# Kernel tuning notes

Hardware: AMD Instinct MI355X
Metric: run time of the kernel (lower is better)

The kernel has to match this reference:

```python
import jax, jax.numpy as jnp
import numpy as np

NUM_EMBEDDINGS = 8192
EMBEDDING_DIM = 256


def setup_inputs() -> dict:
    key = jax.random.key(0)
    k1, k2 = jax.random.split(key)
    z = jax.random.normal(k1, (8, 4096, EMBEDDING_DIM), dtype=jnp.float32)
    # stand-in for orthogonally-initialized nn.Embedding weight
    codebook = jax.random.normal(k2, (NUM_EMBEDDINGS, EMBEDDING_DIM), dtype=jnp.float32)
    return {"z": z, "codebook": codebook}


def reference(z, codebook):
    # z: [..., D], codebook: [K, D]
    zf = z.reshape(-1, EMBEDDING_DIM)                      # [N, D]
    # squared-euclidean distances via ||z||^2 + ||e||^2 - 2 z.e^T
    distances = (
        jnp.sum(zf * zf, axis=1, keepdims=True)            # [N, 1]
        + jnp.sum(codebook * codebook, axis=1)             # [K]
        - 2.0 * jnp.matmul(zf, codebook.T)                 # [N, K]
    )
    encoding_indices = jnp.argmin(distances, axis=1)[:, None]  # [N, 1]
    quantized = codebook[encoding_indices[:, 0]]           # [N, D] gather
    quantized = quantized.reshape(z.shape)
    return quantized, encoding_indices
```

## Files before the change

### kernel.cpp

```cpp
#include <hip/hip_runtime.h>
#include <cfloat>
#include <stdint.h>

#define NROWS   32768
#define NCODES  8192
#define KDIM    256
#define QOUT_OFFSET (NROWS * KDIM)

#define BM      64
#define BN      256
#define NQ      4
#define CODES_Q (NCODES / NQ)
#define NKC     (KDIM / 32)
#define NIT     (CODES_Q / BN * NKC)
#define THREADS 256

#define BPAN 8192
#define BBUF (2 * BPAN)
#define ALDS_SPLIT 32768

typedef __bf16 bf16x4 __attribute__((ext_vector_type(4)));
typedef __bf16 bf16x8 __attribute__((ext_vector_type(8)));
typedef float  f32x4  __attribute__((ext_vector_type(4)));

__global__ void vq_panel_kernel(const float* __restrict__ cb,
                                char* __restrict__ cbP,
                                float* __restrict__ cnorm) {
    const int t    = threadIdx.x;
    const int row  = t >> 2;
    const int seg  = t & 3;
    const int code = blockIdx.x * 64 + row;
    const int cl   = code & 127;
    const int pt   = code >> 7;
    const float4* cb4 = (const float4*)cb;

    float ssq = 0.f;
    #pragma unroll
    for (int i = 0; i < 16; ++i) {
        int f = seg * 16 + i;
        float4 v = cb4[(size_t)code * 64 + f];
        int k   = f * 4;
        int kc  = k >> 5;
        int kl  = k & 31;
        int oct = kl >> 3;
        int rem = kl & 7;
        bf16x4 h, l;
        float xs[4] = {v.x, v.y, v.z, v.w};
        #pragma unroll
        for (int e = 0; e < 4; ++e) {
            __bf16 hh = (__bf16)xs[e];
            h[e] = hh;
            l[e] = (__bf16)(xs[e] - (float)hh);
            ssq  = fmaf(xs[e], xs[e], ssq);
        }
        int lanefrag = (oct << 4) | (cl & 15);
        char* base = cbP + ((size_t)(pt * NKC + kc)) * BBUF
                         + ((cl >> 4) * 64 + lanefrag) * 16 + rem * 2;
        *(bf16x4*)base          = h;
        *(bf16x4*)(base + BPAN) = l;
    }
    ssq += __shfl_xor(ssq, 1, 64);
    ssq += __shfl_xor(ssq, 2, 64);
    if (seg == 0) cnorm[code] = ssq;
}

__global__ __launch_bounds__(THREADS, 2) void vq_main_kernel(
        const float* __restrict__ z, const char* __restrict__ cbP,
        const float* __restrict__ cnorm,
        float* __restrict__ partD, int* __restrict__ partI) {

    __shared__ __align__(16) char Alds[2 * ALDS_SPLIT];

    const int t     = threadIdx.x;
    const int wave  = t >> 6;
    const int lane  = t & 63;
    const int l15   = lane & 15;
    const int q     = blockIdx.x >> 9;
    const int row0  = (blockIdx.x & 511) * BM;
    const int qcode = q * CODES_Q;
    const int qp16  = q * 16;

    const float4* z4 = (const float4*)z;

    f32x4 acc[4][4];
    float mv[16];
    int   mi[16];
    #pragma unroll
    for (int i = 0; i < 4; ++i)
        #pragma unroll
        for (int j = 0; j < 4; ++j)
            acc[i][j] = (f32x4){0.f, 0.f, 0.f, 0.f};
    #pragma unroll
    for (int s = 0; s < 16; ++s) { mv[s] = FLT_MAX; mi[s] = 0; }

    {
        const int arow = t >> 2;
        const int aseg = t & 3;
        #pragma unroll
        for (int p = 0; p < 8; ++p) {
            float4 f0 = z4[(size_t)(row0 + arow) * 64 + aseg * 16 + 2 * p];
            float4 f1 = z4[(size_t)(row0 + arow) * 64 + aseg * 16 + 2 * p + 1];
            float xs[8] = {f0.x, f0.y, f0.z, f0.w, f1.x, f1.y, f1.z, f1.w};
            bf16x8 hv, lv;
            #pragma unroll
            for (int e = 0; e < 8; ++e) {
                __bf16 hh = (__bf16)xs[e];
                hv[e] = hh;
                lv[e] = (__bf16)(xs[e] - (float)hh);
            }
            int kc  = aseg * 2 + (p >> 2);
            int oct = p & 3;
            int slot = ((kc * 4 + (arow >> 4)) * 64 + (oct << 4) + (arow & 15)) * 16;
            *(bf16x8*)(Alds + slot)              = hv;
            *(bf16x8*)(Alds + ALDS_SPLIT + slot) = lv;
        }
    }

    bf16x8 B0h[4], B0l[4], B1h[4], B1l[4];
    #pragma unroll
    for (int j = 0; j < 4; ++j) {
        int g16 = wave * 4 + j;
        const char* pb = cbP + ((size_t)(qp16 + (g16 >> 3)) * 8 + 0) * BBUF
                             + ((g16 & 7) * 64 + lane) * 16;
        B0h[j] = *(const bf16x8*)pb;
        B0l[j] = *(const bf16x8*)(pb + BPAN);
    }

    __syncthreads();

#define VQ_BODY(N, CURH, CURL, NXTH, NXTL)                                    \
    {                                                                         \
        const int ct = (N) >> 3, kc = (N) & 7;                                \
        const int np = (N) + 1;                                               \
        if (np < NIT) {                                                       \
            const int ct1 = np >> 3, kc1 = np & 7;                            \
            _Pragma("unroll")                                                 \
            for (int j = 0; j < 4; ++j) {                                     \
                int g16 = ct1 * 16 + wave * 4 + j;                            \
                const char* pb = cbP                                          \
                    + ((size_t)(qp16 + (g16 >> 3)) * 8 + kc1) * BBUF          \
                    + ((g16 & 7) * 64 + lane) * 16;                           \
                NXTH[j] = *(const bf16x8*)pb;                                 \
                NXTL[j] = *(const bf16x8*)(pb + BPAN);                        \
            }                                                                 \
        }                                                                     \
        bf16x8 ah[4], al[4];                                                  \
        _Pragma("unroll")                                                     \
        for (int i = 0; i < 4; ++i) {                                         \
            int sl = ((kc * 4 + i) * 64 + lane) * 16;                         \
            ah[i] = *(const bf16x8*)(Alds + sl);                              \
            al[i] = *(const bf16x8*)(Alds + ALDS_SPLIT + sl);                 \
        }                                                                     \
        _Pragma("unroll")                                                     \
        for (int i = 0; i < 4; ++i)                                           \
            _Pragma("unroll")                                                 \
            for (int j = 0; j < 4; ++j)                                       \
                acc[i][j] = __builtin_amdgcn_mfma_f32_16x16x32_bf16(          \
                                ah[i], CURH[j], acc[i][j], 0, 0, 0);          \
        _Pragma("unroll")                                                     \
        for (int i = 0; i < 4; ++i)                                           \
            _Pragma("unroll")                                                 \
            for (int j = 0; j < 4; ++j)                                       \
                acc[i][j] = __builtin_amdgcn_mfma_f32_16x16x32_bf16(          \
                                ah[i], CURL[j], acc[i][j], 0, 0, 0);          \
        _Pragma("unroll")                                                     \
        for (int i = 0; i < 4; ++i)                                           \
            _Pragma("unroll")                                                 \
            for (int j = 0; j < 4; ++j)                                       \
                acc[i][j] = __builtin_amdgcn_mfma_f32_16x16x32_bf16(          \
                                al[i], CURH[j], acc[i][j], 0, 0, 0);          \
        if (kc == 7) {                                                        \
            _Pragma("unroll")                                                 \
            for (int j = 0; j < 4; ++j) {                                     \
                int code = qcode + (ct * 16 + wave * 4 + j) * 16 + l15;       \
                float cn = cnorm[code];                                       \
                _Pragma("unroll")                                             \
                for (int i = 0; i < 4; ++i) {                                 \
                    _Pragma("unroll")                                         \
                    for (int r = 0; r < 4; ++r) {                             \
                        float d = fmaf(-2.f, acc[i][j][r], cn);               \
                        int s = i * 4 + r;                                    \
                        if (d < mv[s]) { mv[s] = d; mi[s] = code; }           \
                    }                                                         \
                    acc[i][j] = (f32x4){0.f, 0.f, 0.f, 0.f};                  \
                }                                                             \
            }                                                                 \
        }                                                                     \
    }

    for (int n = 0; n < NIT; n += 2) {
        VQ_BODY(n,     B0h, B0l, B1h, B1l)
        VQ_BODY(n + 1, B1h, B1l, B0h, B0l)
    }
#undef VQ_BODY

    #pragma unroll
    for (int s = 0; s < 16; ++s) {
        #pragma unroll
        for (int m = 1; m <= 8; m <<= 1) {
            float ov = __shfl_xor(mv[s], m, 64);
            int   oi = __shfl_xor(mi[s], m, 64);
            if (ov < mv[s] || (ov == mv[s] && oi < mi[s])) { mv[s] = ov; mi[s] = oi; }
        }
    }
    __syncthreads();
    float* redV = (float*)Alds;
    int*   redI = (int*)(Alds + 4 * BM * 4);
    if (l15 == 0) {
        int qq = lane >> 4;
        #pragma unroll
        for (int i = 0; i < 4; ++i)
            #pragma unroll
            for (int r = 0; r < 4; ++r) {
                int ml = i * 16 + qq * 4 + r;
                redV[wave * BM + ml] = mv[i * 4 + r];
                redI[wave * BM + ml] = mi[i * 4 + r];
            }
    }
    __syncthreads();
    if (t < BM) {
        float bv = redV[t];
        int   bi = redI[t];
        #pragma unroll
        for (int w = 1; w < 4; ++w) {
            float v  = redV[w * BM + t];
            int   id = redI[w * BM + t];
            if (v < bv || (v == bv && id < bi)) { bv = v; bi = id; }
        }
        partD[(size_t)q * NROWS + row0 + t] = bv;
        partI[(size_t)q * NROWS + row0 + t] = bi;
    }
}

__global__ void vq_merge_kernel(const float* __restrict__ partD,
                                const int* __restrict__ partI,
                                float* __restrict__ idx_out) {
    const int row = blockIdx.x * 256 + threadIdx.x;
    float bv = partD[row];
    int   bi = partI[row];
    #pragma unroll
    for (int q = 1; q < NQ; ++q) {
        float v  = partD[(size_t)q * NROWS + row];
        int   id = partI[(size_t)q * NROWS + row];
        if (v < bv || (v == bv && id < bi)) { bv = v; bi = id; }
    }
    idx_out[row] = (float)bi;
}

__global__ void vq_gather_kernel(const float* __restrict__ cb,
                                 const float* __restrict__ idx_f,
                                 float* __restrict__ quant) {
    const int t   = threadIdx.x;
    const int row = blockIdx.x * 64 + (t >> 2);
    const int seg = t & 3;
    const int best = (int)idx_f[row];
    const float4* src = (const float4*)cb + (size_t)best * (KDIM / 4);
    float4* dst = (float4*)quant + (size_t)row * (KDIM / 4);
    #pragma unroll
    for (int i = 0; i < 16; ++i)
        dst[seg * 16 + i] = src[seg * 16 + i];
}

extern "C" void kernel_launch(void* const* d_in, const int* in_sizes, int n_in,
                              void* d_out, int out_size, void* d_ws, size_t ws_size,
                              hipStream_t stream) {
    const float* z  = (const float*)d_in[0];
    const float* cb = (const float*)d_in[1];
    float* quant   = (float*)d_out;
    float* idx_out = (float*)d_out + QOUT_OFFSET;
    float* cnorm   = (float*)d_ws;
    char*  cbP     = (char*)d_out;
    float* partD   = (float*)((char*)d_out + 8 * 1024 * 1024);
    int*   partI   = (int*)((char*)d_out + 8 * 1024 * 1024 + NQ * NROWS * 4);

    vq_panel_kernel<<<NCODES / 64, 256, 0, stream>>>(cb, cbP, cnorm);
    vq_main_kernel<<<NQ * (NROWS / BM), THREADS, 0, stream>>>(z, cbP, cnorm, partD, partI);
    vq_merge_kernel<<<NROWS / 256, 256, 0, stream>>>(partD, partI, idx_out);
    vq_gather_kernel<<<NROWS / 64, 256, 0, stream>>>(cb, idx_out, quant);
}
```

Measured before the change: 423.7 us.

## Double-buffer A fragments from LDS and prefetch codebook norms early

```diff
diff --git a/kernel.cpp b/kernel.cpp
--- a/kernel.cpp
+++ b/kernel.cpp
@@ -79,6 +79,8 @@
     const int row0  = (blockIdx.x & 511) * BM;
     const int qcode = q * CODES_Q;
     const int qp16  = q * 16;
+    const int wp    = wave >> 1;
+    const int bvoff = ((wave & 1) * 256 + lane) * 16;
 
     const float4* z4 = (const float4*)z;
 
@@ -117,63 +119,84 @@
     }
 
     bf16x8 B0h[4], B0l[4], B1h[4], B1l[4];
-    #pragma unroll
-    for (int j = 0; j < 4; ++j) {
-        int g16 = wave * 4 + j;
-        const char* pb = cbP + ((size_t)(qp16 + (g16 >> 3)) * 8 + 0) * BBUF
-                             + ((g16 & 7) * 64 + lane) * 16;
-        B0h[j] = *(const bf16x8*)pb;
-        B0l[j] = *(const bf16x8*)(pb + BPAN);
+    {
+        const char* pb  = cbP + ((size_t)(qp16 + wp) * 8) * BBUF + bvoff;
+        const char* pbl = pb + BPAN;
+        #pragma unroll
+        for (int j = 0; j < 4; ++j) {
+            B0h[j] = *(const bf16x8*)(pb  + j * 1024);
+            B0l[j] = *(const bf16x8*)(pbl + j * 1024);
+        }
     }
 
     __syncthreads();
 
-#define VQ_BODY(N, CURH, CURL, NXTH, NXTL)                                    \
+    bf16x8 A0h[4], A0l[4], A1h[4], A1l[4];
+    {
+        const char* ab = Alds + (lane << 4);
+        #pragma unroll
+        for (int i = 0; i < 4; ++i) {
+            A0h[i] = *(const bf16x8*)(ab + i * 1024);
+            A0l[i] = *(const bf16x8*)(ab + ALDS_SPLIT + i * 1024);
+        }
+    }
+
+    float cnj[4];
+
+#define VQ_BODY(N, CAH, CAL, NAH, NAL, CBH, CBL, NBH, NBL)                    \
     {                                                                         \
         const int ct = (N) >> 3, kc = (N) & 7;                                \
         const int np = (N) + 1;                                               \
         if (np < NIT) {                                                       \
             const int ct1 = np >> 3, kc1 = np & 7;                            \
+            const char* pb  = cbP                                             \
+                + ((size_t)((qp16 + ct1 * 2 + wp) * 8 + kc1)) * BBUF + bvoff; \
+            const char* pbl = pb + BPAN;                                      \
             _Pragma("unroll")                                                 \
             for (int j = 0; j < 4; ++j) {                                     \
-                int g16 = ct1 * 16 + wave * 4 + j;                            \
-                const char* pb = cbP                                          \
-                    + ((size_t)(qp16 + (g16 >> 3)) * 8 + kc1) * BBUF          \
-                    + ((g16 & 7) * 64 + lane) * 16;                           \
-                NXTH[j] = *(const bf16x8*)pb;                                 \
-                NXTL[j] = *(const bf16x8*)(pb + BPAN);                        \
+                NBH[j] = *(const bf16x8*)(pb  + j * 1024);                    \
+                NBL[j] = *(const bf16x8*)(pbl + j * 1024);                    \
             }                                                                 \
         }                                                                     \
-        bf16x8 ah[4], al[4];                                                  \
-        _Pragma("unroll")                                                     \
-        for (int i = 0; i < 4; ++i) {                                         \
-            int sl = ((kc * 4 + i) * 64 + lane) * 16;                         \
-            ah[i] = *(const bf16x8*)(Alds + sl);                              \
-            al[i] = *(const bf16x8*)(Alds + ALDS_SPLIT + sl);                 \
+        {                                                                     \
+            const int kcn = np & 7;                                           \
+            const char* ab = Alds + (kcn << 12) + (lane << 4);                \
+            _Pragma("unroll")                                                 \
+            for (int i = 0; i < 4; ++i) {                                     \
+                NAH[i] = *(const bf16x8*)(ab + i * 1024);                     \
+                NAL[i] = *(const bf16x8*)(ab + ALDS_SPLIT + i * 1024);        \
+            }                                                                 \
         }                                                                     \
+        if (kc == 0) {                                                        \
+            _Pragma("unroll")                                                 \
+            for (int j = 0; j < 4; ++j)                                       \
+                cnj[j] = cnorm[qcode + (ct * 16 + wave * 4 + j) * 16 + l15];  \
+        }                                                                     \
+        __builtin_amdgcn_s_setprio(1);                                        \
         _Pragma("unroll")                                                     \
         for (int i = 0; i < 4; ++i)                                           \
             _Pragma("unroll")                                                 \
             for (int j = 0; j < 4; ++j)                                       \
                 acc[i][j] = __builtin_amdgcn_mfma_f32_16x16x32_bf16(          \
-                                ah[i], CURH[j], acc[i][j], 0, 0, 0);          \
+                                CAH[i], CBH[j], acc[i][j], 0, 0, 0);          \
         _Pragma("unroll")                                                     \
         for (int i = 0; i < 4; ++i)                                           \
             _Pragma("unroll")                                                 \
             for (int j = 0; j < 4; ++j)                                       \
                 acc[i][j] = __builtin_amdgcn_mfma_f32_16x16x32_bf16(          \
-                                ah[i], CURL[j], acc[i][j], 0, 0, 0);          \
+                                CAH[i], CBL[j], acc[i][j], 0, 0, 0);          \
         _Pragma("unroll")                                                     \
         for (int i = 0; i < 4; ++i)                                           \
             _Pragma("unroll")                                                 \
             for (int j = 0; j < 4; ++j)                                       \
                 acc[i][j] = __builtin_amdgcn_mfma_f32_16x16x32_bf16(          \
-                                al[i], CURH[j], acc[i][j], 0, 0, 0);          \
+                                CAL[i], CBH[j], acc[i][j], 0, 0, 0);          \
+        __builtin_amdgcn_s_setprio(0);                                        \
         if (kc == 7) {                                                        \
             _Pragma("unroll")                                                 \
             for (int j = 0; j < 4; ++j) {                                     \
                 int code = qcode + (ct * 16 + wave * 4 + j) * 16 + l15;       \
-                float cn = cnorm[code];                                       \
+                float cn = cnj[j];                                            \
                 _Pragma("unroll")                                             \
                 for (int i = 0; i < 4; ++i) {                                 \
                     _Pragma("unroll")                                         \
@@ -189,8 +212,8 @@
     }
 
     for (int n = 0; n < NIT; n += 2) {
-        VQ_BODY(n,     B0h, B0l, B1h, B1l)
-        VQ_BODY(n + 1, B1h, B1l, B0h, B0l)
+        VQ_BODY(n,     A0h, A0l, A1h, A1l, B0h, B0l, B1h, B1l)
+        VQ_BODY(n + 1, A1h, A1l, A0h, A0l, B1h, B1l, B0h, B0l)
     }
 #undef VQ_BODY
 
```

Measured after the change: 422.3 us. No clear change (-0.3%).

## Switch distance GEMM to 32x32x16 MFMA with new panel layout and setprio

Applied to the files above, without the earlier changes.

```diff
diff --git a/kernel.cpp b/kernel.cpp
--- a/kernel.cpp
+++ b/kernel.cpp
@@ -11,8 +11,6 @@
 #define BN      256
 #define NQ      4
 #define CODES_Q (NCODES / NQ)
-#define NKC     (KDIM / 32)
-#define NIT     (CODES_Q / BN * NKC)
 #define THREADS 256
 
 #define BPAN 8192
@@ -21,7 +19,7 @@
 
 typedef __bf16 bf16x4 __attribute__((ext_vector_type(4)));
 typedef __bf16 bf16x8 __attribute__((ext_vector_type(8)));
-typedef float  f32x4  __attribute__((ext_vector_type(4)));
+typedef float  f32x16 __attribute__((ext_vector_type(16)));
 
 __global__ void vq_panel_kernel(const float* __restrict__ cb,
                                 char* __restrict__ cbP,
@@ -39,23 +37,23 @@
     for (int i = 0; i < 16; ++i) {
         int f = seg * 16 + i;
         float4 v = cb4[(size_t)code * 64 + f];
-        int k   = f * 4;
-        int kc  = k >> 5;
-        int kl  = k & 31;
-        int oct = kl >> 3;
-        int rem = kl & 7;
+        int k  = f * 4;
+        int kc = k >> 5;
+        int s  = (k >> 4) & 1;
+        int g  = (k >> 3) & 1;
+        int e  = k & 7;
         bf16x4 h, l;
         float xs[4] = {v.x, v.y, v.z, v.w};
         #pragma unroll
-        for (int e = 0; e < 4; ++e) {
-            __bf16 hh = (__bf16)xs[e];
-            h[e] = hh;
-            l[e] = (__bf16)(xs[e] - (float)hh);
-            ssq  = fmaf(xs[e], xs[e], ssq);
-        }
-        int lanefrag = (oct << 4) | (cl & 15);
-        char* base = cbP + ((size_t)(pt * NKC + kc)) * BBUF
-                         + ((cl >> 4) * 64 + lanefrag) * 16 + rem * 2;
+        for (int e2 = 0; e2 < 4; ++e2) {
+            __bf16 hh = (__bf16)xs[e2];
+            h[e2] = hh;
+            l[e2] = (__bf16)(xs[e2] - (float)hh);
+            ssq  = fmaf(xs[e2], xs[e2], ssq);
+        }
+        int lane = (g << 5) | (code & 31);
+        char* base = cbP + (size_t)(pt * 8 + kc) * BBUF
+                   + (((cl >> 5) * 2 + s) * 64 + lane) * 16 + e * 2;
         *(bf16x4*)base          = h;
         *(bf16x4*)(base + BPAN) = l;
     }
@@ -74,28 +72,34 @@
     const int t     = threadIdx.x;
     const int wave  = t >> 6;
     const int lane  = t & 63;
-    const int l15   = lane & 15;
+    const int l31   = lane & 31;
     const int q     = blockIdx.x >> 9;
     const int row0  = (blockIdx.x & 511) * BM;
     const int qcode = q * CODES_Q;
     const int qp16  = q * 16;
+    const int wh    = wave >> 1;
+    const int wboff = (wave & 1) * 4096 + lane * 16;
 
     const float4* z4 = (const float4*)z;
 
-    f32x4 acc[4][4];
-    float mv[16];
-    int   mi[16];
-    #pragma unroll
-    for (int i = 0; i < 4; ++i)
-        #pragma unroll
-        for (int j = 0; j < 4; ++j)
-            acc[i][j] = (f32x4){0.f, 0.f, 0.f, 0.f};
-    #pragma unroll
-    for (int s = 0; s < 16; ++s) { mv[s] = FLT_MAX; mi[s] = 0; }
+    f32x16 acc[2][2];
+    float mv[32];
+    int   mi[32];
+    #pragma unroll
+    for (int i = 0; i < 2; ++i)
+        #pragma unroll
+        for (int j = 0; j < 2; ++j)
+            #pragma unroll
+            for (int r = 0; r < 16; ++r)
+                acc[i][j][r] = 0.f;
+    #pragma unroll
+    for (int s = 0; s < 32; ++s) { mv[s] = FLT_MAX; mi[s] = 0; }
 
     {
         const int arow = t >> 2;
         const int aseg = t & 3;
+        const int ai   = arow >> 5;
+        const int al31 = arow & 31;
         #pragma unroll
         for (int p = 0; p < 8; ++p) {
             float4 f0 = z4[(size_t)(row0 + arow) * 64 + aseg * 16 + 2 * p];
@@ -108,113 +112,132 @@
                 hv[e] = hh;
                 lv[e] = (__bf16)(xs[e] - (float)hh);
             }
-            int kc  = aseg * 2 + (p >> 2);
-            int oct = p & 3;
-            int slot = ((kc * 4 + (arow >> 4)) * 64 + (oct << 4) + (arow & 15)) * 16;
+            int kc = aseg * 2 + (p >> 2);
+            int s  = (p >> 1) & 1;
+            int g  = p & 1;
+            int slot = kc * 4096 + ai * 2048 + s * 1024 + ((g << 5) | al31) * 16;
             *(bf16x8*)(Alds + slot)              = hv;
             *(bf16x8*)(Alds + ALDS_SPLIT + slot) = lv;
         }
     }
 
+    const char* pct = cbP + (size_t)(qp16 + wh) * 8 * BBUF + wboff;
     bf16x8 B0h[4], B0l[4], B1h[4], B1l[4];
     #pragma unroll
-    for (int j = 0; j < 4; ++j) {
-        int g16 = wave * 4 + j;
-        const char* pb = cbP + ((size_t)(qp16 + (g16 >> 3)) * 8 + 0) * BBUF
-                             + ((g16 & 7) * 64 + lane) * 16;
-        B0h[j] = *(const bf16x8*)pb;
-        B0l[j] = *(const bf16x8*)(pb + BPAN);
+    for (int js = 0; js < 4; ++js) {
+        B0h[js] = *(const bf16x8*)(pct + js * 1024);
+        B0l[js] = *(const bf16x8*)(pct + BPAN + js * 1024);
     }
 
     __syncthreads();
 
-#define VQ_BODY(N, CURH, CURL, NXTH, NXTL)                                    \
+    const char* ab = (const char*)Alds + (lane << 4);
+    float cnj[2];
+
+#define VQ_KC(KC, NOFF, PREF, CBH, CBL, NBH, NBL)                             \
     {                                                                         \
-        const int ct = (N) >> 3, kc = (N) & 7;                                \
-        const int np = (N) + 1;                                               \
-        if (np < NIT) {                                                       \
-            const int ct1 = np >> 3, kc1 = np & 7;                            \
+        if (PREF) {                                                           \
+            const char* pn  = pct + (size_t)(NOFF) * BBUF;                    \
             _Pragma("unroll")                                                 \
-            for (int j = 0; j < 4; ++j) {                                     \
-                int g16 = ct1 * 16 + wave * 4 + j;                            \
-                const char* pb = cbP                                          \
-                    + ((size_t)(qp16 + (g16 >> 3)) * 8 + kc1) * BBUF          \
-                    + ((g16 & 7) * 64 + lane) * 16;                           \
-                NXTH[j] = *(const bf16x8*)pb;                                 \
-                NXTL[j] = *(const bf16x8*)(pb + BPAN);                        \
+            for (int js = 0; js < 4; ++js) {                                  \
+                NBH[js] = *(const bf16x8*)(pn + js * 1024);                   \
+                NBL[js] = *(const bf16x8*)(pn + BPAN + js * 1024);            \
             }                                                                 \
         }                                                                     \
         bf16x8 ah[4], al[4];                                                  \
         _Pragma("unroll")                                                     \
-        for (int i = 0; i < 4; ++i) {                                         \
-            int sl = ((kc * 4 + i) * 64 + lane) * 16;                         \
-            ah[i] = *(const bf16x8*)(Alds + sl);                              \
-            al[i] = *(const bf16x8*)(Alds + ALDS_SPLIT + sl);                 \
+        for (int is = 0; is < 4; ++is) {                                      \
+            ah[is] = *(const bf16x8*)(ab + (KC) * 4096 + is * 1024);          \
+            al[is] = *(const bf16x8*)(ab + ALDS_SPLIT + (KC) * 4096 + is * 1024); \
         }                                                                     \
+        __builtin_amdgcn_s_setprio(1);                                        \
         _Pragma("unroll")                                                     \
-        for (int i = 0; i < 4; ++i)                                           \
+        for (int i = 0; i < 2; ++i)                                           \
             _Pragma("unroll")                                                 \
-            for (int j = 0; j < 4; ++j)                                       \
-                acc[i][j] = __builtin_amdgcn_mfma_f32_16x16x32_bf16(          \
-                                ah[i], CURH[j], acc[i][j], 0, 0, 0);          \
+            for (int j = 0; j < 2; ++j)                                       \
+                _Pragma("unroll")                                             \
+                for (int s = 0; s < 2; ++s)                                   \
+                    acc[i][j] = __builtin_amdgcn_mfma_f32_32x32x16_bf16(      \
+                        ah[i * 2 + s], CBH[j * 2 + s], acc[i][j], 0, 0, 0);   \
         _Pragma("unroll")                                                     \
-        for (int i = 0; i < 4; ++i)                                           \
+        for (int i = 0; i < 2; ++i)                                           \
             _Pragma("unroll")                                                 \
-            for (int j = 0; j < 4; ++j)                                       \
-                acc[i][j] = __builtin_amdgcn_mfma_f32_16x16x32_bf16(          \
-                                ah[i], CURL[j], acc[i][j], 0, 0, 0);          \
+            for (int j = 0; j < 2; ++j)                                       \
+                _Pragma("unroll")                                             \
+                for (int s = 0; s < 2; ++s)                                   \
+                    acc[i][j] = __builtin_amdgcn_mfma_f32_32x32x16_bf16(      \
+                        ah[i * 2 + s], CBL[j * 2 + s], acc[i][j], 0, 0, 0);   \
         _Pragma("unroll")                                                     \
-        for (int i = 0; i < 4; ++i)                                           \
+        for (int i = 0; i < 2; ++i)                                           \
             _Pragma("unroll")                                                 \
-            for (int j = 0; j < 4; ++j)                                       \
-                acc[i][j] = __builtin_amdgcn_mfma_f32_16x16x32_bf16(          \
-                                al[i], CURH[j], acc[i][j], 0, 0, 0);          \
-        if (kc == 7) {                                                        \
-            _Pragma("unroll")                                                 \
-            for (int j = 0; j < 4; ++j) {                                     \
-                int code = qcode + (ct * 16 + wave * 4 + j) * 16 + l15;       \
-                float cn = cnorm[code];                                       \
+            for (int j = 0; j < 2; ++j)                                       \
                 _Pragma("unroll")                                             \
-                for (int i = 0; i < 4; ++i) {                                 \
-                    _Pragma("unroll")                                         \
-                    for (int r = 0; r < 4; ++r) {                             \
-                        float d = fmaf(-2.f, acc[i][j][r], cn);               \
-                        int s = i * 4 + r;                                    \
-                        if (d < mv[s]) { mv[s] = d; mi[s] = code; }           \
-                    }                                                         \
-                    acc[i][j] = (f32x4){0.f, 0.f, 0.f, 0.f};                  \
-                }                                                             \
-            }                                                                 \
-        }                                                                     \
-    }
-
-    for (int n = 0; n < NIT; n += 2) {
-        VQ_BODY(n,     B0h, B0l, B1h, B1l)
-        VQ_BODY(n + 1, B1h, B1l, B0h, B0l)
-    }
-#undef VQ_BODY
-
-    #pragma unroll
-    for (int s = 0; s < 16; ++s) {
-        #pragma unroll
-        for (int m = 1; m <= 8; m <<= 1) {
-            float ov = __shfl_xor(mv[s], m, 64);
-            int   oi = __shfl_xor(mi[s], m, 64);
-            if (ov < mv[s] || (ov == mv[s] && oi < mi[s])) { mv[s] = ov; mi[s] = oi; }
+                for (int s = 0; s < 2; ++s)                                   \
+                    acc[i][j] = __builtin_amdgcn_mfma_f32_32x32x16_bf16(      \
+                        al[i * 2 + s], CBH[j * 2 + s], acc[i][j], 0, 0, 0);   \
+        __builtin_amdgcn_s_setprio(0);                                        \
+    }
+
+    for (int ct = 0; ct < 8; ++ct) {
+        #pragma unroll
+        for (int j = 0; j < 2; ++j)
+            cnj[j] = cnorm[qcode + ct * 256 + wave * 64 + j * 32 + l31];
+        const bool morect = (ct < 7);
+        VQ_KC(0, 1,  true,   B0h, B0l, B1h, B1l)
+        VQ_KC(1, 2,  true,   B1h, B1l, B0h, B0l)
+        VQ_KC(2, 3,  true,   B0h, B0l, B1h, B1l)
+        VQ_KC(3, 4,  true,   B1h, B1l, B0h, B0l)
+        VQ_KC(4, 5,  true,   B0h, B0l, B1h, B1l)
+        VQ_KC(5, 6,  true,   B1h, B1l, B0h, B0l)
+        VQ_KC(6, 7,  true,   B0h, B0l, B1h, B1l)
+        VQ_KC(7, 16, morect, B1h, B1l, B0h, B0l)
+
+        #pragma unroll
+        for (int j = 0; j < 2; ++j) {
+            const float cn  = cnj[j];
+            const int  code = qcode + ct * 256 + wave * 64 + j * 32 + l31;
+            #pragma unroll
+            for (int i = 0; i < 2; ++i)
+                #pragma unroll
+                for (int r = 0; r < 16; ++r) {
+                    float d = fmaf(-2.f, acc[i][j][r], cn);
+                    const int sl = i * 16 + r;
+                    if (d < mv[sl]) { mv[sl] = d; mi[sl] = code; }
+                }
+        }
+        #pragma unroll
+        for (int i = 0; i < 2; ++i)
+            #pragma unroll
+            for (int j = 0; j < 2; ++j)
+                #pragma unroll
+                for (int r = 0; r < 16; ++r)
+                    acc[i][j][r] = 0.f;
+
+        pct += (size_t)16 * BBUF;
+    }
+#undef VQ_KC
+
+    #pragma unroll
+    for (int sl = 0; sl < 32; ++sl) {
+        #pragma unroll
+        for (int m = 1; m <= 16; m <<= 1) {
+            float ov = __shfl_xor(mv[sl], m, 64);
+            int   oi = __shfl_xor(mi[sl], m, 64);
+            if (ov < mv[sl] || (ov == mv[sl] && oi < mi[sl])) { mv[sl] = ov; mi[sl] = oi; }
         }
     }
     __syncthreads();
     float* redV = (float*)Alds;
     int*   redI = (int*)(Alds + 4 * BM * 4);
-    if (l15 == 0) {
-        int qq = lane >> 4;
-        #pragma unroll
-        for (int i = 0; i < 4; ++i)
-            #pragma unroll
-            for (int r = 0; r < 4; ++r) {
-                int ml = i * 16 + qq * 4 + r;
-                redV[wave * BM + ml] = mv[i * 4 + r];
-                redI[wave * BM + ml] = mi[i * 4 + r];
+    if (l31 == 0) {
+        const int hi = lane >> 5;
+        #pragma unroll
+        for (int i = 0; i < 2; ++i)
+            #pragma unroll
+            for (int r = 0; r < 16; ++r) {
+                int rowl = i * 32 + (r & 3) + 8 * (r >> 2) + 4 * hi;
+                redV[wave * BM + rowl] = mv[i * 16 + r];
+                redI[wave * BM + rowl] = mi[i * 16 + r];
             }
     }
     __syncthreads();
```

Result: slower. 975.9 us (+130.3%).
